# Optimization experiments

Measured on AMD Instinct MI355X. Metric: run time of the kernel, lower is better.

Reference implementation:

```python
import jax, jax.numpy as jnp
import numpy as np

N_VN = 8000
N_CN = 4000
DV = 3
DC = 6
BATCH = 1250
CODERATE = 0.5
NUM_ITER = 5
LLR_MAX = 20.0
EPS = 1e-12


def _build_graph():
    # regular (3,6) Tanner graph: 3 layers, each layer gives every VN one edge
    # and every CN two edges (n = 2m).
    rng = np.random.RandomState(0)
    vn = np.tile(np.arange(N_VN, dtype=np.int32), DV)
    cn_layers = []
    for _ in range(DV):
        cn_layers.append(rng.permutation(np.repeat(np.arange(N_CN, dtype=np.int32), 2)))
    cn = np.concatenate(cn_layers)
    return vn, cn


def setup_inputs() -> dict:
    key = jax.random.key(0)
    k1, = jax.random.split(key, 1)
    vn, cn = _build_graph()
    noise = jax.random.normal(k1, (BATCH, N_VN), dtype=jnp.float32)
    weights = jnp.ones((DV * N_VN,), dtype=jnp.float32)  # trainable edge weights, init 1
    return {
        "noise": noise,
        "weights": weights,
        "vn_idx": jnp.asarray(vn),
        "cn_idx": jnp.asarray(cn),
        "ebno_db": 4,
    }


def _bp_forward(noise, weights, vn_idx, cn_idx, ebno_db):
    B, n = noise.shape
    m = n // 2
    # ebnodb2no with 1 bit/symbol
    no = 1.0 / (10.0 ** (ebno_db / 10.0) * CODERATE)
    sigma2 = 4.0 / no
    # GaussianPriorSource: llr = log(p(x=1)/p(x=0)) for all-zero codeword
    llr = (-sigma2 / 2.0) + jnp.sqrt(sigma2) * noise  # [B, n]
    # decoder works internally with log(p0/p1); messages kept as [E, B]
    L = -llr.T  # [n, B]
    msg_vn = L[vn_idx]  # [E, B] initial VN->CN messages
    w = weights[:, None]

    loss = jnp.float32(0.0)
    c_hat = None
    for _ in range(NUM_ITER):
        # ---- check node update (boxplus, leave-one-out in log domain) ----
        mw = jnp.clip(msg_vn * w, -LLR_MAX, LLR_MAX)
        t = jnp.tanh(mw / 2.0)  # [E, B]
        log_t = jnp.log(jnp.maximum(jnp.abs(t), EPS))
        neg = (t < 0).astype(jnp.float32)
        sum_log = jax.ops.segment_sum(log_t, cn_idx, num_segments=m)  # [m, B]
        sum_neg = jax.ops.segment_sum(neg, cn_idx, num_segments=m)
        parity = jnp.mod(sum_neg[cn_idx] - neg, 2.0)
        sign = 1.0 - 2.0 * parity
        mag = jnp.exp(sum_log[cn_idx] - log_t)
        prod = jnp.clip(sign * mag, -1.0 + 1e-7, 1.0 - 1e-7)
        msg_cn = 2.0 * jnp.arctanh(prod)  # [E, B] CN->VN messages
        # ---- variable node update + marginalization ----
        x_tot = L + jax.ops.segment_sum(msg_cn, vn_idx, num_segments=n)  # [n, B]
        msg_vn = x_tot[vn_idx] - msg_cn
        c_hat = -x_tot.T  # back to log(p1/p0) convention, [B, n]
        # BCE(from_logits) with all-zero labels -> mean softplus(logits)
        loss = loss + jnp.mean(jax.nn.softplus(c_hat))
    loss = loss / NUM_ITER
    c = jnp.zeros((B, n), dtype=jnp.float32)
    return c, c_hat, llr, loss


def reference(noise, weights, vn_idx, cn_idx, ebno_db):
    return _bp_forward(noise, weights, vn_idx, cn_idx, ebno_db)
```

## Files before the change

### kernel.cpp

```cpp
#include <hip/hip_runtime.h>
#include <hip/hip_fp16.h>
#include <math.h>

constexpr int N_VN   = 8000;
constexpr int N_CN   = 4000;
constexpr int DV     = 3;
constexpr int DC     = 6;
constexpr int EDGES  = N_VN * DV;
constexpr int BATCH  = 1250;
constexpr int NUM_ITER = 5;
constexpr int NBLK   = 250;
constexpr float LLR_MAX = 20.0f;
constexpr float MSGMAX = 16.635532f;
constexpr float FFLOOR = 2e-12f;
constexpr float QSCALE = 32767.0f / 20.0f;
constexpr float QINV   = 20.0f / 32767.0f;
constexpr float LOG2E  = 1.44269504f;
constexpr float LN2    = 0.69314718f;
constexpr float C3     = QSCALE * LN2;
constexpr float QMSGMAX = MSGMAX * QSCALE;

constexpr int MTPB  = 1024;
constexpr int VREM  = N_VN - 7 * MTPB;
constexpr int CREM  = N_CN - 3 * MTPB;

__device__ __forceinline__ unsigned pack_sex2(float mv0, float mv1, float w) {
    float mw0 = fminf(fmaxf(mv0 * w, -LLR_MAX), LLR_MAX);
    float mw1 = fminf(fmaxf(mv1 * w, -LLR_MAX), LLR_MAX);
    float e0 = exp2f(-fabsf(mw0) * LOG2E);
    float e1 = exp2f(-fabsf(mw1) * LOG2E);
    float s0 = __uint_as_float(__float_as_uint(e0) | (__float_as_uint(mw0) & 0x80000000u));
    float s1 = __uint_as_float(__float_as_uint(e1) | (__float_as_uint(mw1) & 0x80000000u));
    auto hp = __builtin_amdgcn_cvt_pkrtz(s0, s1);
    unsigned u;
    __builtin_memcpy(&u, &hp, 4);
    return u;
}

__device__ __forceinline__ float half_bits_to_f32(unsigned short hbits) {
    return __half2float(__ushort_as_half(hbits));
}

__device__ __forceinline__ float pack_ex(float mv, float w) {
    float mw = fminf(fmaxf(mv * w, -LLR_MAX), LLR_MAX);
    float ex = exp2f(-fabsf(mw) * LOG2E);
    return __uint_as_float(__float_as_uint(ex) | (__float_as_uint(mw) & 0x80000000u));
}

__global__ __launch_bounds__(MTPB, 4) void bp_mega_k(const float* __restrict__ noise,
                                                     const float* __restrict__ weights,
                                                     const int* __restrict__ cn_idx,
                                                     const int* __restrict__ ebno,
                                                     float* __restrict__ llr_out,
                                                     float* __restrict__ chat_out,
                                                     float* __restrict__ c_out,
                                                     float* __restrict__ loss_part) {
    __shared__ unsigned eSu[EDGES];
    __shared__ float hs[2];
    __shared__ float red[MTPB / 64];

    const int tid  = threadIdx.x;
    const int base = blockIdx.x * 5;

    if (tid == 0) {
        double sig2 = 2.0 * pow(10.0, (double)ebno[0] * 0.1);
        hs[0] = (float)(sig2 * 0.5);
        hs[1] = (float)sqrt(sig2);
    }

    int*            cnt   = (int*)eSu;
    unsigned short* eposS = (unsigned short*)(eSu + 4000);
    #pragma unroll
    for (int k = 0; k < 4; ++k) {
        int i = tid + k * MTPB;
        if (k < 3 || tid < CREM) cnt[i] = 0;
    }
    __syncthreads();
    for (int e = tid; e < EDGES; e += MTPB) {
        int c = cn_idx[e];
        int slot = atomicAdd(&cnt[c], 1);
        eposS[e] = (unsigned short)(slot * N_CN + c);
    }
    __syncthreads();
    int   pp[8][DV];
    float wt[8][DV];
    #pragma unroll
    for (int r = 0; r < 8; ++r) {
        int v = tid + r * MTPB;
        if (r < 7 || tid < VREM) {
            #pragma unroll
            for (int l = 0; l < DV; ++l) {
                pp[r][l] = eposS[v + l * N_VN];
                wt[r][l] = weights[v + l * N_VN];
            }
        }
    }
    const float h = hs[0], s = hs[1];

    float spMax = 0.0f, spLog = 0.0f;

    auto run_pair = [&](int b0i, int b1i) {
        const float* nrow0 = noise    + (size_t)b0i * N_VN;
        const float* nrow1 = noise    + (size_t)b1i * N_VN;
        float*       lrow0 = llr_out  + (size_t)b0i * N_VN;
        float*       lrow1 = llr_out  + (size_t)b1i * N_VN;
        float*       crow0 = chat_out + (size_t)b0i * N_VN;
        float*       crow1 = chat_out + (size_t)b1i * N_VN;
        float*       zrow0 = c_out    + (size_t)b0i * N_VN;
        float*       zrow1 = c_out    + (size_t)b1i * N_VN;
        float L0[8], L1[8];
        __syncthreads();
        #pragma unroll
        for (int r = 0; r < 8; ++r) {
            int v = tid + r * MTPB;
            if (r < 7 || tid < VREM) {
                float n0 = nrow0[v], n1 = nrow1[v];
                float llr0 = fmaf(s, n0, -h), llr1 = fmaf(s, n1, -h);
                lrow0[v] = llr0; lrow1[v] = llr1;
                zrow0[v] = 0.0f; zrow1[v] = 0.0f;
                L0[r] = -llr0; L1[r] = -llr1;
                #pragma unroll
                for (int l = 0; l < DV; ++l)
                    eSu[pp[r][l]] = pack_sex2(L0[r], L1[r], wt[r][l]);
            }
        }
        #pragma unroll 1
        for (int it = 0; it < NUM_ITER; ++it) {
            __syncthreads();
            #pragma unroll
            for (int k = 0; k < 4; ++k) {
                int c = tid + k * MTPB;
                if (k < 3 || tid < CREM) {
                    unsigned d[DC];
                    float f0[DC], f1[DC];
                    float na0 = 1.0f, nb0 = 1.0f, da0 = 1.0f, db0 = 1.0f;
                    float na1 = 1.0f, nb1 = 1.0f, da1 = 1.0f, db1 = 1.0f;
                    unsigned sx = 0u;
                    #pragma unroll
                    for (int j = 0; j < DC; ++j) {
                        d[j] = eSu[c + j * N_CN];
                        sx ^= d[j];
                        float s0 = half_bits_to_f32((unsigned short)d[j]);
                        float s1 = half_bits_to_f32((unsigned short)(d[j] >> 16));
                        float F0 = fmaxf(1.0f - fabsf(s0), FFLOOR);
                        float F1 = fmaxf(1.0f - fabsf(s1), FFLOOR);
                        f0[j] = F0; f1[j] = F1;
                        if (j & 1) { nb0 *= F0; db0 *= (2.0f - F0);
                                     nb1 *= F1; db1 *= (2.0f - F1); }
                        else       { na0 *= F0; da0 *= (2.0f - F0);
                                     na1 *= F1; da1 *= (2.0f - F1); }
                    }
                    float T0 = __fdividef(na0 * nb0, da0 * db0);
                    float T1 = __fdividef(na1 * nb1, da1 * db1);
                    #pragma unroll
                    for (int j = 0; j < DC; ++j) {
                        float g0 = T0 * (2.0f - f0[j]);
                        float g1 = T1 * (2.0f - f1[j]);
                        float r0 = __fdividef(f0[j] + g0, f0[j] - g0);
                        float r1 = __fdividef(f1[j] + g1, f1[j] - g1);
                        float q0 = fminf(__log2f(r0) * C3, QMSGMAX);
                        float q1 = fminf(__log2f(r1) * C3, QMSGMAX);
                        unsigned sp = sx ^ d[j];
                        float m0 = __uint_as_float(__float_as_uint(q0) ^ ((sp & 0x8000u) << 16));
                        float m1 = __uint_as_float(__float_as_uint(q1) ^ (sp & 0x80000000u));
                        int i0 = __float2int_rn(m0);
                        int i1 = __float2int_rn(m1);
                        eSu[c + j * N_CN] = ((unsigned)i0 & 0xffffu) | ((unsigned)i1 << 16);
                    }
                }
            }
            __syncthreads();
            const bool wr = (it != NUM_ITER - 1);
            #pragma unroll
            for (int r = 0; r < 8; ++r) {
                int v = tid + r * MTPB;
                if (r < 7 || tid < VREM) {
                    unsigned da = eSu[pp[r][0]];
                    unsigned db = eSu[pp[r][1]];
                    unsigned dc = eSu[pp[r][2]];
                    int a0 = (int)(short)da, a1 = (int)da >> 16;
                    int b0 = (int)(short)db, b1 = (int)db >> 16;
                    int c0 = (int)(short)dc, c1 = (int)dc >> 16;
                    float xt0 = fmaf((float)(a0 + b0 + c0), QINV, L0[r]);
                    float xt1 = fmaf((float)(a1 + b1 + c1), QINV, L1[r]);
                    if (wr) {
                        float ma0 = fmaf((float)a0, -QINV, xt0);
                        float ma1 = fmaf((float)a1, -QINV, xt1);
                        float mb0 = fmaf((float)b0, -QINV, xt0);
                        float mb1 = fmaf((float)b1, -QINV, xt1);
                        float mc0 = fmaf((float)c0, -QINV, xt0);
                        float mc1 = fmaf((float)c1, -QINV, xt1);
                        eSu[pp[r][0]] = pack_sex2(ma0, ma1, wt[r][0]);
                        eSu[pp[r][1]] = pack_sex2(mb0, mb1, wt[r][1]);
                        eSu[pp[r][2]] = pack_sex2(mc0, mc1, wt[r][2]);
                    } else {
                        crow0[v] = -xt0;
                        crow1[v] = -xt1;
                    }
                    spMax += fmaxf(-xt0, 0.0f) + fmaxf(-xt1, 0.0f);
                    spLog += __log2f(1.0f + exp2f(-fabsf(xt0) * LOG2E));
                    spLog += __log2f(1.0f + exp2f(-fabsf(xt1) * LOG2E));
                }
            }
        }
    };

    auto run_single = [&](int b0i) {
        float* eSf = (float*)eSu;
        const float* nrow = noise    + (size_t)b0i * N_VN;
        float*       lrow = llr_out  + (size_t)b0i * N_VN;
        float*       crow = chat_out + (size_t)b0i * N_VN;
        float*       zrow = c_out    + (size_t)b0i * N_VN;
        float Lr[8];
        __syncthreads();
        #pragma unroll
        for (int r = 0; r < 8; ++r) {
            int v = tid + r * MTPB;
            if (r < 7 || tid < VREM) {
                float nv  = nrow[v];
                float llr = fmaf(s, nv, -h);
                lrow[v] = llr;
                zrow[v] = 0.0f;
                Lr[r] = -llr;
                #pragma unroll
                for (int l = 0; l < DV; ++l)
                    eSf[pp[r][l]] = pack_ex(Lr[r], wt[r][l]);
            }
        }
        #pragma unroll 1
        for (int it = 0; it < NUM_ITER; ++it) {
            __syncthreads();
            #pragma unroll
            for (int k = 0; k < 4; ++k) {
                int c = tid + k * MTPB;
                if (k < 3 || tid < CREM) {
                    float se[DC], f[DC];
                    float na = 1.0f, nb = 1.0f, da = 1.0f, db = 1.0f;
                    unsigned sx = 0u;
                    #pragma unroll
                    for (int j = 0; j < DC; ++j) {
                        se[j] = eSf[c + j * N_CN];
                        float F = fmaxf(1.0f - fabsf(se[j]), FFLOOR);
                        f[j] = F;
                        if (j & 1) { nb *= F; db *= (2.0f - F); }
                        else       { na *= F; da *= (2.0f - F); }
                        sx ^= __float_as_uint(se[j]);
                    }
                    float T = __fdividef(na * nb, da * db);
                    #pragma unroll
                    for (int j = 0; j < DC; ++j) {
                        float g  = T * (2.0f - f[j]);
                        float rr = __fdividef(f[j] + g, f[j] - g);
                        float ma = fminf(__log2f(rr) * LN2, MSGMAX);
                        unsigned sg = (sx ^ __float_as_uint(se[j])) & 0x80000000u;
                        eSf[c + j * N_CN] = __uint_as_float(__float_as_uint(ma) ^ sg);
                    }
                }
            }
            __syncthreads();
            const bool wr = (it != NUM_ITER - 1);
            #pragma unroll
            for (int r = 0; r < 8; ++r) {
                int v = tid + r * MTPB;
                if (r < 7 || tid < VREM) {
                    float m0 = eSf[pp[r][0]];
                    float m1 = eSf[pp[r][1]];
                    float m2 = eSf[pp[r][2]];
                    float xt = Lr[r] + m0 + m1 + m2;
                    if (wr) {
                        eSf[pp[r][0]] = pack_ex(xt - m0, wt[r][0]);
                        eSf[pp[r][1]] = pack_ex(xt - m1, wt[r][1]);
                        eSf[pp[r][2]] = pack_ex(xt - m2, wt[r][2]);
                    } else {
                        crow[v] = -xt;
                    }
                    spMax += fmaxf(-xt, 0.0f);
                    spLog += __log2f(1.0f + exp2f(-fabsf(xt) * LOG2E));
                }
            }
        }
    };

    run_pair(base, base + 1);
    run_pair(base + 2, base + 3);
    run_single(base + 4);

    float lossacc = fmaf(LN2, spLog, spMax);

    #pragma unroll
    for (int off = 32; off > 0; off >>= 1)
        lossacc += __shfl_down(lossacc, off, 64);
    int lane = tid & 63, wid = tid >> 6;
    if (lane == 0) red[wid] = lossacc;
    __syncthreads();
    if (tid == 0) {
        float ssum = 0.0f;
        #pragma unroll
        for (int i = 0; i < MTPB / 64; ++i) ssum += red[i];
        loss_part[blockIdx.x] = ssum;
    }
}

__global__ __launch_bounds__(256) void loss_final_k(const float* __restrict__ lp,
                                                    float* __restrict__ out_loss) {
    double s = 0.0;
    for (int i = threadIdx.x; i < NBLK; i += 256) s += (double)lp[i];
    #pragma unroll
    for (int off = 32; off > 0; off >>= 1)
        s += __shfl_down(s, off, 64);
    __shared__ double red[4];
    int lane = threadIdx.x & 63, wid = threadIdx.x >> 6;
    if (lane == 0) red[wid] = s;
    __syncthreads();
    if (threadIdx.x == 0)
        out_loss[0] = (float)((red[0] + red[1] + red[2] + red[3]) /
                              ((double)NUM_ITER * (double)BATCH * (double)N_VN));
}

extern "C" void kernel_launch(void* const* d_in, const int* in_sizes, int n_in,
                              void* d_out, int out_size, void* d_ws, size_t ws_size,
                              hipStream_t stream) {
    const float* noise   = (const float*)d_in[0];
    const float* weights = (const float*)d_in[1];
    const int* cn_idx    = (const int*)d_in[3];
    const int* ebno      = (const int*)d_in[4];

    float* out      = (float*)d_out;
    float* out_c    = out;
    float* out_chat = out + 10000000;
    float* out_llr  = out + 20000000;
    float* out_loss = out + 30000000;

    float* loss_part = (float*)d_ws;

    bp_mega_k<<<dim3(NBLK), dim3(MTPB), 0, stream>>>(noise, weights, cn_idx, ebno,
                                                     out_llr, out_chat, out_c, loss_part);

    loss_final_k<<<dim3(1), dim3(256), 0, stream>>>(loss_part, out_loss);
}
```

Measured before the change: 392.5 us.

## Move edge position table to LDS and shrink register footprint of BP loops

The per-thread edge-position register array is replaced by a separate LDS table. The first CN pass's stored f/d arrays are dropped: the second pass re-reads each message from LDS and recomputes its term. The CN and VN loops get unroll 1 and the min-blocks launch-bounds hint is removed. The aim is to cut register pressure, at the cost of extra LDS reads and 48KB more LDS. The VN loops still index the register arrays wt, L0/L1 and Lr with a runtime r, which can push them to scratch memory.

```diff
diff --git a/kernel.cpp b/kernel.cpp
--- a/kernel.cpp
+++ b/kernel.cpp
@@ -47,15 +47,16 @@
     return __uint_as_float(__float_as_uint(ex) | (__float_as_uint(mw) & 0x80000000u));
 }
 
-__global__ __launch_bounds__(MTPB, 4) void bp_mega_k(const float* __restrict__ noise,
-                                                     const float* __restrict__ weights,
-                                                     const int* __restrict__ cn_idx,
-                                                     const int* __restrict__ ebno,
-                                                     float* __restrict__ llr_out,
-                                                     float* __restrict__ chat_out,
-                                                     float* __restrict__ c_out,
-                                                     float* __restrict__ loss_part) {
-    __shared__ unsigned eSu[EDGES];
+__global__ __launch_bounds__(MTPB) void bp_mega_k(const float* __restrict__ noise,
+                                                  const float* __restrict__ weights,
+                                                  const int* __restrict__ cn_idx,
+                                                  const int* __restrict__ ebno,
+                                                  float* __restrict__ llr_out,
+                                                  float* __restrict__ chat_out,
+                                                  float* __restrict__ c_out,
+                                                  float* __restrict__ loss_part) {
+    __shared__ unsigned       eSu[EDGES];
+    __shared__ unsigned short eposL[EDGES];
     __shared__ float hs[2];
     __shared__ float red[MTPB / 64];
 
@@ -68,8 +69,7 @@
         hs[1] = (float)sqrt(sig2);
     }
 
-    int*            cnt   = (int*)eSu;
-    unsigned short* eposS = (unsigned short*)(eSu + 4000);
+    int* cnt = (int*)eSu;
     #pragma unroll
     for (int k = 0; k < 4; ++k) {
         int i = tid + k * MTPB;
@@ -79,22 +79,19 @@
     for (int e = tid; e < EDGES; e += MTPB) {
         int c = cn_idx[e];
         int slot = atomicAdd(&cnt[c], 1);
-        eposS[e] = (unsigned short)(slot * N_CN + c);
-    }
-    __syncthreads();
-    int   pp[8][DV];
+        eposL[e] = (unsigned short)(slot * N_CN + c);
+    }
     float wt[8][DV];
     #pragma unroll
     for (int r = 0; r < 8; ++r) {
         int v = tid + r * MTPB;
         if (r < 7 || tid < VREM) {
             #pragma unroll
-            for (int l = 0; l < DV; ++l) {
-                pp[r][l] = eposS[v + l * N_VN];
+            for (int l = 0; l < DV; ++l)
                 wt[r][l] = weights[v + l * N_VN];
-            }
-        }
-    }
+        }
+    }
+    __syncthreads();
     const float h = hs[0], s = hs[1];
 
     float spMax = 0.0f, spLog = 0.0f;
@@ -121,30 +118,25 @@
                 L0[r] = -llr0; L1[r] = -llr1;
                 #pragma unroll
                 for (int l = 0; l < DV; ++l)
-                    eSu[pp[r][l]] = pack_sex2(L0[r], L1[r], wt[r][l]);
+                    eSu[eposL[v + l * N_VN]] = pack_sex2(L0[r], L1[r], wt[r][l]);
             }
         }
         #pragma unroll 1
         for (int it = 0; it < NUM_ITER; ++it) {
             __syncthreads();
-            #pragma unroll
+            #pragma unroll 1
             for (int k = 0; k < 4; ++k) {
                 int c = tid + k * MTPB;
                 if (k < 3 || tid < CREM) {
-                    unsigned d[DC];
-                    float f0[DC], f1[DC];
                     float na0 = 1.0f, nb0 = 1.0f, da0 = 1.0f, db0 = 1.0f;
                     float na1 = 1.0f, nb1 = 1.0f, da1 = 1.0f, db1 = 1.0f;
                     unsigned sx = 0u;
                     #pragma unroll
                     for (int j = 0; j < DC; ++j) {
-                        d[j] = eSu[c + j * N_CN];
-                        sx ^= d[j];
-                        float s0 = half_bits_to_f32((unsigned short)d[j]);
-                        float s1 = half_bits_to_f32((unsigned short)(d[j] >> 16));
-                        float F0 = fmaxf(1.0f - fabsf(s0), FFLOOR);
-                        float F1 = fmaxf(1.0f - fabsf(s1), FFLOOR);
-                        f0[j] = F0; f1[j] = F1;
+                        unsigned d = eSu[c + j * N_CN];
+                        sx ^= d;
+                        float F0 = fmaxf(1.0f - fabsf(half_bits_to_f32((unsigned short)d)), FFLOOR);
+                        float F1 = fmaxf(1.0f - fabsf(half_bits_to_f32((unsigned short)(d >> 16))), FFLOOR);
                         if (j & 1) { nb0 *= F0; db0 *= (2.0f - F0);
                                      nb1 *= F1; db1 *= (2.0f - F1); }
                         else       { na0 *= F0; da0 *= (2.0f - F0);
@@ -154,13 +146,16 @@
                     float T1 = __fdividef(na1 * nb1, da1 * db1);
                     #pragma unroll
                     for (int j = 0; j < DC; ++j) {
-                        float g0 = T0 * (2.0f - f0[j]);
-                        float g1 = T1 * (2.0f - f1[j]);
-                        float r0 = __fdividef(f0[j] + g0, f0[j] - g0);
-                        float r1 = __fdividef(f1[j] + g1, f1[j] - g1);
+                        unsigned d = eSu[c + j * N_CN];
+                        float F0 = fmaxf(1.0f - fabsf(half_bits_to_f32((unsigned short)d)), FFLOOR);
+                        float F1 = fmaxf(1.0f - fabsf(half_bits_to_f32((unsigned short)(d >> 16))), FFLOOR);
+                        float g0 = T0 * (2.0f - F0);
+                        float g1 = T1 * (2.0f - F1);
+                        float r0 = __fdividef(F0 + g0, F0 - g0);
+                        float r1 = __fdividef(F1 + g1, F1 - g1);
                         float q0 = fminf(__log2f(r0) * C3, QMSGMAX);
                         float q1 = fminf(__log2f(r1) * C3, QMSGMAX);
-                        unsigned sp = sx ^ d[j];
+                        unsigned sp = sx ^ d;
                         float m0 = __uint_as_float(__float_as_uint(q0) ^ ((sp & 0x8000u) << 16));
                         float m1 = __uint_as_float(__float_as_uint(q1) ^ (sp & 0x80000000u));
                         int i0 = __float2int_rn(m0);
@@ -171,13 +166,16 @@
             }
             __syncthreads();
             const bool wr = (it != NUM_ITER - 1);
-            #pragma unroll
+            #pragma unroll 1
             for (int r = 0; r < 8; ++r) {
                 int v = tid + r * MTPB;
                 if (r < 7 || tid < VREM) {
-                    unsigned da = eSu[pp[r][0]];
-                    unsigned db = eSu[pp[r][1]];
-                    unsigned dc = eSu[pp[r][2]];
+                    int p0 = eposL[v];
+                    int p1 = eposL[v + N_VN];
+                    int p2 = eposL[v + 2 * N_VN];
+                    unsigned da = eSu[p0];
+                    unsigned db = eSu[p1];
+                    unsigned dc = eSu[p2];
                     int a0 = (int)(short)da, a1 = (int)da >> 16;
                     int b0 = (int)(short)db, b1 = (int)db >> 16;
                     int c0 = (int)(short)dc, c1 = (int)dc >> 16;
@@ -190,9 +188,9 @@
                         float mb1 = fmaf((float)b1, -QINV, xt1);
                         float mc0 = fmaf((float)c0, -QINV, xt0);
                         float mc1 = fmaf((float)c1, -QINV, xt1);
-                        eSu[pp[r][0]] = pack_sex2(ma0, ma1, wt[r][0]);
-                        eSu[pp[r][1]] = pack_sex2(mb0, mb1, wt[r][1]);
-                        eSu[pp[r][2]] = pack_sex2(mc0, mc1, wt[r][2]);
+                        eSu[p0] = pack_sex2(ma0, ma1, wt[r][0]);
+                        eSu[p1] = pack_sex2(mb0, mb1, wt[r][1]);
+                        eSu[p2] = pack_sex2(mc0, mc1, wt[r][2]);
                     } else {
                         crow0[v] = -xt0;
                         crow1[v] = -xt1;
@@ -224,53 +222,56 @@
                 Lr[r] = -llr;
                 #pragma unroll
                 for (int l = 0; l < DV; ++l)
-                    eSf[pp[r][l]] = pack_ex(Lr[r], wt[r][l]);
+                    eSf[eposL[v + l * N_VN]] = pack_ex(Lr[r], wt[r][l]);
             }
         }
         #pragma unroll 1
         for (int it = 0; it < NUM_ITER; ++it) {
             __syncthreads();
-            #pragma unroll
+            #pragma unroll 1
             for (int k = 0; k < 4; ++k) {
                 int c = tid + k * MTPB;
                 if (k < 3 || tid < CREM) {
-                    float se[DC], f[DC];
                     float na = 1.0f, nb = 1.0f, da = 1.0f, db = 1.0f;
                     unsigned sx = 0u;
                     #pragma unroll
                     for (int j = 0; j < DC; ++j) {
-                        se[j] = eSf[c + j * N_CN];
-                        float F = fmaxf(1.0f - fabsf(se[j]), FFLOOR);
-                        f[j] = F;
+                        float se = eSf[c + j * N_CN];
+                        float F = fmaxf(1.0f - fabsf(se), FFLOOR);
                         if (j & 1) { nb *= F; db *= (2.0f - F); }
                         else       { na *= F; da *= (2.0f - F); }
-                        sx ^= __float_as_uint(se[j]);
+                        sx ^= __float_as_uint(se);
                     }
                     float T = __fdividef(na * nb, da * db);
                     #pragma unroll
                     for (int j = 0; j < DC; ++j) {
-                        float g  = T * (2.0f - f[j]);
-                        float rr = __fdividef(f[j] + g, f[j] - g);
+                        float se = eSf[c + j * N_CN];
+                        float F = fmaxf(1.0f - fabsf(se), FFLOOR);
+                        float g  = T * (2.0f - F);
+                        float rr = __fdividef(F + g, F - g);
                         float ma = fminf(__log2f(rr) * LN2, MSGMAX);
-                        unsigned sg = (sx ^ __float_as_uint(se[j])) & 0x80000000u;
+                        unsigned sg = (sx ^ __float_as_uint(se)) & 0x80000000u;
                         eSf[c + j * N_CN] = __uint_as_float(__float_as_uint(ma) ^ sg);
                     }
                 }
             }
             __syncthreads();
             const bool wr = (it != NUM_ITER - 1);
-            #pragma unroll
+            #pragma unroll 1
             for (int r = 0; r < 8; ++r) {
                 int v = tid + r * MTPB;
                 if (r < 7 || tid < VREM) {
-                    float m0 = eSf[pp[r][0]];
-                    float m1 = eSf[pp[r][1]];
-                    float m2 = eSf[pp[r][2]];
+                    int p0 = eposL[v];
+                    int p1 = eposL[v + N_VN];
+                    int p2 = eposL[v + 2 * N_VN];
+                    float m0 = eSf[p0];
+                    float m1 = eSf[p1];
+                    float m2 = eSf[p2];
                     float xt = Lr[r] + m0 + m1 + m2;
                     if (wr) {
-                        eSf[pp[r][0]] = pack_ex(xt - m0, wt[r][0]);
-                        eSf[pp[r][1]] = pack_ex(xt - m1, wt[r][1]);
-                        eSf[pp[r][2]] = pack_ex(xt - m2, wt[r][2]);
+                        eSf[p0] = pack_ex(xt - m0, wt[r][0]);
+                        eSf[p1] = pack_ex(xt - m1, wt[r][1]);
+                        eSf[p2] = pack_ex(xt - m2, wt[r][2]);
                     } else {
                         crow[v] = -xt;
                     }
```

Result: faster. 378.7 us (-3.5%).
